# Kernel tuning notes

Hardware: AMD Instinct MI355X
Metric: run time of the kernel (lower is better)

## Reference

```python
import jax, jax.numpy as jnp
import numpy as np

N_CODEBOOKS = 4
N_EMBED = 1024
EMBED_DIM = 64
PATCH = 4
BETA = 0.25
EPS = 1e-5
USAGE_W = 0.01


def setup_inputs() -> dict:
    key = jax.random.key(0)
    k1, k2 = jax.random.split(key)
    z = jax.random.normal(k1, (8, 64, 128, 128), dtype=jnp.float32)
    # one EMA codebook per quantizer, initialized ~ randn like torch buffer
    codebooks = jax.random.normal(k2, (N_CODEBOOKS, N_EMBED, EMBED_DIM), dtype=jnp.float32)
    return {"z": z, "codebooks": codebooks}


def _usage_loss(indices, n_embed):
    # negative-entropy penalty on code usage (no gradient path: counts are ints)
    counts = jnp.bincount(indices.reshape(-1), length=n_embed).astype(jnp.float32)
    probs = (counts + EPS) / (counts.sum() + EPS * n_embed)
    entropy = -jnp.sum(probs * jnp.log(probs + EPS))
    return jnp.log(jnp.float32(n_embed)) - entropy


def _ema_quantize(residual, embedding):
    # residual: [N, C, ph, pw], embedding: [n_e, C]; eval mode (no EMA buffer update)
    N, C, ph, pw = residual.shape
    z_flat = residual.transpose(0, 2, 3, 1).reshape(-1, C)  # [M, C]
    d = (jnp.sum(z_flat ** 2, axis=1, keepdims=True)
         + jnp.sum(embedding ** 2, axis=1)
         - 2.0 * z_flat @ embedding.T)  # [M, n_e]
    idx = jnp.argmin(d, axis=1)  # [M]
    z_q = embedding[idx].reshape(N, ph, pw, C).transpose(0, 3, 1, 2)  # [N, C, ph, pw]
    loss = BETA * jnp.mean((jax.lax.stop_gradient(z_q) - residual) ** 2)
    z_q_st = residual + jax.lax.stop_gradient(z_q - residual)  # straight-through
    return z_q_st, loss, idx.reshape(N, ph, pw)


def reference(z, codebooks):
    B, C, H, W = z.shape
    h, w = H // PATCH, W // PATCH
    # b c (h ph) (w pw) -> (b h w) c ph pw
    zp = (z.reshape(B, C, h, PATCH, w, PATCH)
            .transpose(0, 2, 4, 1, 3, 5)
            .reshape(B * h * w, C, PATCH, PATCH))
    zq_acc = jnp.zeros_like(zp)
    residual = zp
    losses, all_idx = [], []
    for i in range(N_CODEBOOKS):
        zq_i, loss_i, idx_i = _ema_quantize(residual, codebooks[i])
        loss_i = loss_i + USAGE_W * _usage_loss(idx_i, N_EMBED)
        zq_acc = zq_acc + zq_i
        residual = residual - zq_i
        losses.append(loss_i)
        all_idx.append(idx_i.reshape(idx_i.shape[0], -1))  # [N, ph*pw]
    loss = jnp.stack(losses).sum()
    # (b h w) c ph pw -> b c (h ph) (w pw)
    z_q = (zq_acc.reshape(B, h, w, C, PATCH, PATCH)
                 .transpose(0, 3, 1, 4, 2, 5)
                 .reshape(B, C, H, W))
    # [N, patch_area, n_codebooks] -> [b, h, w, patch_area, n_codebooks]
    min_idx = jnp.stack(all_idx, axis=-1).reshape(B, h, w, PATCH * PATCH, N_CODEBOOKS)
    return z_q, loss, min_idx
```

## Files before the change

kernel.cpp:

```cpp
#include <hip/hip_runtime.h>
#include <math.h>

typedef __attribute__((ext_vector_type(8))) short short8;
typedef __attribute__((ext_vector_type(4))) float f32x4;

#define NCB 4
#define NE 1024
#define DIM 64
#define HW 16384
#define NPIX 131072
#define NWAVES 4096
#define MSE_DENOM 8388608.0f
#define EPSF 1e-5f

__device__ __forceinline__ unsigned short f2bf(float x) {
    unsigned u = __float_as_uint(x);
    u += 0x7fffu + ((u >> 16) & 1u);
    return (unsigned short)(u >> 16);
}
__device__ __forceinline__ float bf2f(unsigned short h) {
    return __uint_as_float(((unsigned)h) << 16);
}

__global__ __launch_bounds__(64) void rvq_norms(const float* __restrict__ cb,
                                                float* __restrict__ norms) {
    int code = blockIdx.x * 64 + threadIdx.x;
    const float4* row = reinterpret_cast<const float4*>(cb + (size_t)code * DIM);
    float s0 = 0.f, s1 = 0.f, s2 = 0.f, s3 = 0.f;
#pragma unroll
    for (int k = 0; k < 16; ++k) {
        float4 v = row[k];
        s0 = fmaf(v.x, v.x, s0); s1 = fmaf(v.y, v.y, s1);
        s2 = fmaf(v.z, v.z, s2); s3 = fmaf(v.w, v.w, s3);
    }
    norms[code] = (s0 + s1) + (s2 + s3);
}

__global__ __launch_bounds__(256, 2) void rvq_main(
    const float* __restrict__ z, const float* __restrict__ cb,
    const float* __restrict__ norms,
    float* __restrict__ out_zq, float* __restrict__ out_idx,
    unsigned* __restrict__ hist, float* __restrict__ msePartial)
{
    __shared__ unsigned short sB[3 * 4096];
    __shared__ float sN[64];
    __shared__ int   sBest[4][32];

    const int tid  = threadIdx.x;
    const int lane = tid & 63;
    const int wid  = tid >> 6;
    const int col  = lane & 15;
    const int g    = lane >> 4;
    const int blockPix = blockIdx.x * 128;
    char* sBc = reinterpret_cast<char*>(sB);

    int pf[2]; size_t zb[2];
#pragma unroll
    for (int m = 0; m < 2; ++m) {
        pf[m] = blockPix + wid * 32 + m * 16 + col;
        zb[m] = (size_t)(pf[m] >> 14) * 1048576 + (size_t)(pf[m] & 16383);
    }

    float r[2][2][8];
#pragma unroll
    for (int m = 0; m < 2; ++m)
#pragma unroll
        for (int kh = 0; kh < 2; ++kh)
#pragma unroll
            for (int e = 0; e < 8; ++e)
                r[m][kh][e] = z[zb[m] + (size_t)(kh * 32 + g * 8 + e) * HW];

    for (int i = 0; i < NCB; ++i) {
        const float* cbi = cb + (size_t)i * NE * DIM;

        short8 A[3][2][2];
#pragma unroll
        for (int m = 0; m < 2; ++m)
#pragma unroll
            for (int kh = 0; kh < 2; ++kh)
#pragma unroll
                for (int e = 0; e < 8; ++e) {
                    float t = r[m][kh][e];
                    unsigned short u1 = f2bf(t); t -= bf2f(u1);
                    unsigned short u2 = f2bf(t); t -= bf2f(u2);
                    unsigned short u3 = f2bf(t);
                    A[0][m][kh][e] = (short)u1;
                    A[1][m][kh][e] = (short)u2;
                    A[2][m][kh][e] = (short)u3;
                }

        float minv[2][4]; int mini[2][4];
#pragma unroll
        for (int m = 0; m < 2; ++m)
#pragma unroll
            for (int rr = 0; rr < 4; ++rr) { minv[m][rr] = 3.4e38f; mini[m][rr] = 0; }

        for (int c0 = 0; c0 < NE; c0 += 64) {
            __syncthreads();
            {
                int code = tid >> 2, dg = tid & 3;
                const float4* s4 = reinterpret_cast<const float4*>(
                    cbi + (size_t)(c0 + code) * DIM + dg * 16);
                float v[16];
                {
                    float4 q;
                    q = s4[0]; v[0]=q.x; v[1]=q.y; v[2]=q.z; v[3]=q.w;
                    q = s4[1]; v[4]=q.x; v[5]=q.y; v[6]=q.z; v[7]=q.w;
                    q = s4[2]; v[8]=q.x; v[9]=q.y; v[10]=q.z; v[11]=q.w;
                    q = s4[3]; v[12]=q.x; v[13]=q.y; v[14]=q.z; v[15]=q.w;
                }
                int linbase = code * 128 + dg * 32;
                int sw = (code & 7) << 4;
#pragma unroll
                for (int h = 0; h < 2; ++h) {
                    short8 p1, p2, p3;
#pragma unroll
                    for (int e = 0; e < 8; ++e) {
                        float t = v[h * 8 + e];
                        unsigned short u1 = f2bf(t); t -= bf2f(u1);
                        unsigned short u2 = f2bf(t); t -= bf2f(u2);
                        unsigned short u3 = f2bf(t);
                        p1[e] = (short)u1; p2[e] = (short)u2; p3[e] = (short)u3;
                    }
                    int a = (linbase + h * 16) ^ sw;
                    *reinterpret_cast<short8*>(sBc + a)         = p1;
                    *reinterpret_cast<short8*>(sBc + 8192 + a)  = p2;
                    *reinterpret_cast<short8*>(sBc + 16384 + a) = p3;
                }
                if (tid < 64) sN[tid] = norms[i * NE + c0 + tid];
            }
            __syncthreads();

#pragma unroll
            for (int sub = 0; sub < 4; ++sub) {
                int code = sub * 16 + col;
                int sw = (code & 7) << 4;
                short8 B[3][2];
#pragma unroll
                for (int s = 0; s < 3; ++s)
#pragma unroll
                    for (int kh = 0; kh < 2; ++kh) {
                        int a = ((code << 7) + (kh << 6) + (g << 4)) ^ sw;
                        B[s][kh] = *reinterpret_cast<const short8*>(sBc + s * 8192 + a);
                    }
                float nrm = sN[code];
                f32x4 acc[2][2];
#pragma unroll
                for (int m = 0; m < 2; ++m)
#pragma unroll
                    for (int rr = 0; rr < 4; ++rr) {
                        acc[m][0][rr] = -0.5f * nrm;
                        acc[m][1][rr] = 0.f;
                    }
#pragma unroll
                for (int m = 0; m < 2; ++m)
#pragma unroll
                    for (int kh = 0; kh < 2; ++kh) {
                        acc[m][kh] = __builtin_amdgcn_mfma_f32_16x16x32_bf16(A[0][m][kh], B[0][kh], acc[m][kh], 0, 0, 0);
                        acc[m][kh] = __builtin_amdgcn_mfma_f32_16x16x32_bf16(A[0][m][kh], B[1][kh], acc[m][kh], 0, 0, 0);
                        acc[m][kh] = __builtin_amdgcn_mfma_f32_16x16x32_bf16(A[1][m][kh], B[0][kh], acc[m][kh], 0, 0, 0);
                        acc[m][kh] = __builtin_amdgcn_mfma_f32_16x16x32_bf16(A[0][m][kh], B[2][kh], acc[m][kh], 0, 0, 0);
                        acc[m][kh] = __builtin_amdgcn_mfma_f32_16x16x32_bf16(A[1][m][kh], B[1][kh], acc[m][kh], 0, 0, 0);
                        acc[m][kh] = __builtin_amdgcn_mfma_f32_16x16x32_bf16(A[2][m][kh], B[0][kh], acc[m][kh], 0, 0, 0);
                    }
#pragma unroll
                for (int m = 0; m < 2; ++m)
#pragma unroll
                    for (int rr = 0; rr < 4; ++rr) {
                        float dist = -2.0f * (acc[m][0][rr] + acc[m][1][rr]);
                        if (dist < minv[m][rr]) { minv[m][rr] = dist; mini[m][rr] = c0 + code; }
                    }
            }
        }

#pragma unroll
        for (int m = 0; m < 2; ++m)
#pragma unroll
            for (int rr = 0; rr < 4; ++rr) {
                float v = minv[m][rr]; int ix = mini[m][rr];
#pragma unroll
                for (int off = 1; off < 16; off <<= 1) {
                    float ov = __shfl_xor(v, off, 64);
                    int   oi = __shfl_xor(ix, off, 64);
                    if (ov < v || (ov == v && oi < ix)) { v = ov; ix = oi; }
                }
                minv[m][rr] = v; mini[m][rr] = ix;
            }
        __syncthreads();
        if (col == 0) {
#pragma unroll
            for (int m = 0; m < 2; ++m)
#pragma unroll
                for (int rr = 0; rr < 4; ++rr)
                    sBest[wid][m * 16 + g * 4 + rr] = mini[m][rr];
        }
        __syncthreads();
        int best[2];
        best[0] = sBest[wid][col];
        best[1] = sBest[wid][16 + col];

        if (lane < 16) {
#pragma unroll
            for (int m = 0; m < 2; ++m) {
                int pfr = blockPix + wid * 32 + m * 16 + lane;
                int bb = pfr >> 14, yy = (pfr >> 7) & 127, xx = pfr & 127;
                int bi = sBest[wid][m * 16 + lane];
                size_t off = (size_t)bb * 65536 + (size_t)(yy >> 2) * 2048
                           + (size_t)(xx >> 2) * 64
                           + (size_t)(((yy & 3) << 2) + (xx & 3)) * 4 + (size_t)i;
                out_idx[off] = (float)bi;
                atomicAdd(&hist[i * NE + bi], 1u);
            }
        }

#pragma unroll
        for (int m = 0; m < 2; ++m) {
            const float* er = cbi + (size_t)best[m] * DIM;
#pragma unroll
            for (int kh = 0; kh < 2; ++kh) {
                const float4* e4 = reinterpret_cast<const float4*>(er + kh * 32 + g * 8);
                float4 q0 = e4[0], q1 = e4[1];
                r[m][kh][0] -= q0.x; r[m][kh][1] -= q0.y;
                r[m][kh][2] -= q0.z; r[m][kh][3] -= q0.w;
                r[m][kh][4] -= q1.x; r[m][kh][5] -= q1.y;
                r[m][kh][6] -= q1.z; r[m][kh][7] -= q1.w;
            }
        }

        float s = 0.f;
#pragma unroll
        for (int m = 0; m < 2; ++m)
#pragma unroll
            for (int kh = 0; kh < 2; ++kh)
#pragma unroll
                for (int e = 0; e < 8; ++e) s = fmaf(r[m][kh][e], r[m][kh][e], s);
#pragma unroll
        for (int d_ = 32; d_ > 0; d_ >>= 1) s += __shfl_down(s, d_, 64);
        if (lane == 0) msePartial[i * NWAVES + blockIdx.x * 4 + wid] = s;
    }

#pragma unroll
    for (int m = 0; m < 2; ++m)
#pragma unroll
        for (int kh = 0; kh < 2; ++kh)
#pragma unroll
            for (int e = 0; e < 8; ++e) {
                size_t o = zb[m] + (size_t)(kh * 32 + g * 8 + e) * HW;
                out_zq[o] = z[o] - r[m][kh][e];
            }
}

__global__ __launch_bounds__(1024) void rvq_finalize(
    const unsigned* __restrict__ hist, const float* __restrict__ msePartial,
    float* __restrict__ out_loss)
{
    __shared__ float red[1024];
    int t = threadIdx.x;
    float loss = 0.f;
    for (int i = 0; i < NCB; ++i) {
        float cnt = (float)hist[i * NE + t];
        float prob = (cnt + EPSF) / (131072.0f + EPSF * 1024.0f);
        red[t] = -prob * logf(prob + EPSF);
        __syncthreads();
        for (int s = 512; s > 0; s >>= 1) { if (t < s) red[t] += red[t + s]; __syncthreads(); }
        float entropy = red[0];
        __syncthreads();
        red[t] = msePartial[i * NWAVES + t]        + msePartial[i * NWAVES + 1024 + t]
               + msePartial[i * NWAVES + 2048 + t] + msePartial[i * NWAVES + 3072 + t];
        __syncthreads();
        for (int s = 512; s > 0; s >>= 1) { if (t < s) red[t] += red[t + s]; __syncthreads(); }
        float mse_sum = red[0];
        __syncthreads();
        loss += 0.25f * (mse_sum / MSE_DENOM) + 0.01f * (logf(1024.0f) - entropy);
    }
    if (t == 0) out_loss[0] = loss;
}

extern "C" void kernel_launch(void* const* d_in, const int* in_sizes, int n_in,
                              void* d_out, int out_size, void* d_ws, size_t ws_size,
                              hipStream_t stream) {
    const float* z  = (const float*)d_in[0];
    const float* cb = (const float*)d_in[1];

    float* out      = (float*)d_out;
    float* out_zq   = out;
    float* out_loss = out + 8388608;
    float* out_idx  = out + 8388609;

    unsigned* hist       = (unsigned*)d_ws;
    float*    norms      = (float*)((char*)d_ws + 16384);
    float*    msePartial = (float*)((char*)d_ws + 32768);

    hipMemsetAsync(d_ws, 0, 16384, stream);
    rvq_norms<<<64, 64, 0, stream>>>(cb, norms);
    rvq_main<<<1024, 256, 0, stream>>>(z, cb, norms, out_zq, out_idx, hist, msePartial);
    rvq_finalize<<<1, 1024, 0, stream>>>(hist, msePartial, out_loss);
}
```

Measured before the change: 458.8 us.

## Pre-split codebook into bf16 triplets once and double-buffer chunks in LDS

A new pre-pass kernel converts each codebook into three-way bf16 split form in swizzled chunk layout in workspace, so the main kernel no longer redoes the float-to-bf16x3 split for every block. The main kernel copies these prebuilt chunks from global memory into a double-buffered LDS area, prefetching the next chunk into registers while computing on the current one. Norms are pre-scaled by -0.5 and read directly from global memory, and the argmin over distance becomes an argmax over the score. This adds a kernel launch, extra workspace traffic and doubled LDS, which could lower occupancy.

```diff
diff --git a/kernel.cpp b/kernel.cpp
--- a/kernel.cpp
+++ b/kernel.cpp
@@ -12,6 +12,8 @@
 #define NWAVES 4096
 #define MSE_DENOM 8388608.0f
 #define EPSF 1e-5f
+#define CHUNK_BYTES 24576
+#define CHUNK_SHORTS 12288
 
 __device__ __forceinline__ unsigned short f2bf(float x) {
     unsigned u = __float_as_uint(x);
@@ -23,7 +25,7 @@
 }
 
 __global__ __launch_bounds__(64) void rvq_norms(const float* __restrict__ cb,
-                                                float* __restrict__ norms) {
+                                                float* __restrict__ nrmh) {
     int code = blockIdx.x * 64 + threadIdx.x;
     const float4* row = reinterpret_cast<const float4*>(cb + (size_t)code * DIM);
     float s0 = 0.f, s1 = 0.f, s2 = 0.f, s3 = 0.f;
@@ -33,17 +35,54 @@
         s0 = fmaf(v.x, v.x, s0); s1 = fmaf(v.y, v.y, s1);
         s2 = fmaf(v.z, v.z, s2); s3 = fmaf(v.w, v.w, s3);
     }
-    norms[code] = (s0 + s1) + (s2 + s3);
+    nrmh[code] = -0.5f * ((s0 + s1) + (s2 + s3));
+}
+
+__global__ __launch_bounds__(256) void rvq_presplit(const float* __restrict__ cb,
+                                                    unsigned short* __restrict__ gB) {
+    int blk = blockIdx.x;
+    int tid = threadIdx.x;
+    int code = tid >> 2, dg = tid & 3;
+    int c0 = (blk & 15) << 6;
+    int i  = blk >> 4;
+    const float4* s4 = reinterpret_cast<const float4*>(
+        cb + ((size_t)i * NE + c0 + code) * DIM + dg * 16);
+    float v[16];
+    {
+        float4 q;
+        q = s4[0]; v[0]=q.x; v[1]=q.y; v[2]=q.z; v[3]=q.w;
+        q = s4[1]; v[4]=q.x; v[5]=q.y; v[6]=q.z; v[7]=q.w;
+        q = s4[2]; v[8]=q.x; v[9]=q.y; v[10]=q.z; v[11]=q.w;
+        q = s4[3]; v[12]=q.x; v[13]=q.y; v[14]=q.z; v[15]=q.w;
+    }
+    char* outc = reinterpret_cast<char*>(gB + (size_t)blk * CHUNK_SHORTS);
+    int linbase = code * 128 + dg * 32;
+    int sw = (code & 7) << 4;
+#pragma unroll
+    for (int h = 0; h < 2; ++h) {
+        short8 p1, p2, p3;
+#pragma unroll
+        for (int e = 0; e < 8; ++e) {
+            float t = v[h * 8 + e];
+            unsigned short u1 = f2bf(t); t -= bf2f(u1);
+            unsigned short u2 = f2bf(t); t -= bf2f(u2);
+            unsigned short u3 = f2bf(t);
+            p1[e] = (short)u1; p2[e] = (short)u2; p3[e] = (short)u3;
+        }
+        int a = (linbase + h * 16) ^ sw;
+        *reinterpret_cast<short8*>(outc + a)         = p1;
+        *reinterpret_cast<short8*>(outc + 8192 + a)  = p2;
+        *reinterpret_cast<short8*>(outc + 16384 + a) = p3;
+    }
 }
 
 __global__ __launch_bounds__(256, 2) void rvq_main(
-    const float* __restrict__ z, const float* __restrict__ cb,
-    const float* __restrict__ norms,
+    const float* __restrict__ z, const unsigned short* __restrict__ gB,
+    const float* __restrict__ nrmh, const float* __restrict__ cb,
     float* __restrict__ out_zq, float* __restrict__ out_idx,
     unsigned* __restrict__ hist, float* __restrict__ msePartial)
 {
-    __shared__ unsigned short sB[3 * 4096];
-    __shared__ float sN[64];
+    __shared__ uint4 sB[2][CHUNK_BYTES / 16];
     __shared__ int   sBest[4][32];
 
     const int tid  = threadIdx.x;
@@ -52,7 +91,7 @@
     const int col  = lane & 15;
     const int g    = lane >> 4;
     const int blockPix = blockIdx.x * 128;
-    char* sBc = reinterpret_cast<char*>(sB);
+    char* sBase = reinterpret_cast<char*>(sB);
 
     int pf[2]; size_t zb[2];
 #pragma unroll
@@ -71,7 +110,8 @@
                 r[m][kh][e] = z[zb[m] + (size_t)(kh * 32 + g * 8 + e) * HW];
 
     for (int i = 0; i < NCB; ++i) {
-        const float* cbi = cb + (size_t)i * NE * DIM;
+        const char* gBi = reinterpret_cast<const char*>(gB) + (size_t)i * 16 * CHUNK_BYTES;
+        const float* nrm_i = nrmh + i * NE;
 
         short8 A[3][2][2];
 #pragma unroll
@@ -89,51 +129,38 @@
                     A[2][m][kh][e] = (short)u3;
                 }
 
-        float minv[2][4]; int mini[2][4];
+        uint4 st[6];
+#pragma unroll
+        for (int k = 0; k < 6; ++k)
+            st[k] = *reinterpret_cast<const uint4*>(gBi + tid * 16 + k * 4096);
+#pragma unroll
+        for (int k = 0; k < 6; ++k)
+            *reinterpret_cast<uint4*>(sBase + tid * 16 + k * 4096) = st[k];
+        __syncthreads();
+
+        float maxv[2][4]; int maxi[2][4];
 #pragma unroll
         for (int m = 0; m < 2; ++m)
 #pragma unroll
-            for (int rr = 0; rr < 4; ++rr) { minv[m][rr] = 3.4e38f; mini[m][rr] = 0; }
-
-        for (int c0 = 0; c0 < NE; c0 += 64) {
-            __syncthreads();
-            {
-                int code = tid >> 2, dg = tid & 3;
-                const float4* s4 = reinterpret_cast<const float4*>(
-                    cbi + (size_t)(c0 + code) * DIM + dg * 16);
-                float v[16];
-                {
-                    float4 q;
-                    q = s4[0]; v[0]=q.x; v[1]=q.y; v[2]=q.z; v[3]=q.w;
-                    q = s4[1]; v[4]=q.x; v[5]=q.y; v[6]=q.z; v[7]=q.w;
-                    q = s4[2]; v[8]=q.x; v[9]=q.y; v[10]=q.z; v[11]=q.w;
-                    q = s4[3]; v[12]=q.x; v[13]=q.y; v[14]=q.z; v[15]=q.w;
-                }
-                int linbase = code * 128 + dg * 32;
-                int sw = (code & 7) << 4;
-#pragma unroll
-                for (int h = 0; h < 2; ++h) {
-                    short8 p1, p2, p3;
-#pragma unroll
-                    for (int e = 0; e < 8; ++e) {
-                        float t = v[h * 8 + e];
-                        unsigned short u1 = f2bf(t); t -= bf2f(u1);
-                        unsigned short u2 = f2bf(t); t -= bf2f(u2);
-                        unsigned short u3 = f2bf(t);
-                        p1[e] = (short)u1; p2[e] = (short)u2; p3[e] = (short)u3;
-                    }
-                    int a = (linbase + h * 16) ^ sw;
-                    *reinterpret_cast<short8*>(sBc + a)         = p1;
-                    *reinterpret_cast<short8*>(sBc + 8192 + a)  = p2;
-                    *reinterpret_cast<short8*>(sBc + 16384 + a) = p3;
-                }
-                if (tid < 64) sN[tid] = norms[i * NE + c0 + tid];
-            }
-            __syncthreads();
+            for (int rr = 0; rr < 4; ++rr) { maxv[m][rr] = -3.4e38f; maxi[m][rr] = 0; }
+
+        for (int c = 0; c < 16; ++c) {
+            const int cur = c & 1;
+            if (c < 15) {
+                const char* gc = gBi + (size_t)(c + 1) * CHUNK_BYTES;
+#pragma unroll
+                for (int k = 0; k < 6; ++k)
+                    st[k] = *reinterpret_cast<const uint4*>(gc + tid * 16 + k * 4096);
+            }
+            const char* sbc = sBase + cur * CHUNK_BYTES;
+            float nh[4];
+#pragma unroll
+            for (int sub = 0; sub < 4; ++sub)
+                nh[sub] = nrm_i[(c << 6) + (sub << 4) + col];
 
 #pragma unroll
             for (int sub = 0; sub < 4; ++sub) {
-                int code = sub * 16 + col;
+                int code = (sub << 4) + col;
                 int sw = (code & 7) << 4;
                 short8 B[3][2];
 #pragma unroll
@@ -141,15 +168,14 @@
 #pragma unroll
                     for (int kh = 0; kh < 2; ++kh) {
                         int a = ((code << 7) + (kh << 6) + (g << 4)) ^ sw;
-                        B[s][kh] = *reinterpret_cast<const short8*>(sBc + s * 8192 + a);
+                        B[s][kh] = *reinterpret_cast<const short8*>(sbc + s * 8192 + a);
                     }
-                float nrm = sN[code];
                 f32x4 acc[2][2];
 #pragma unroll
                 for (int m = 0; m < 2; ++m)
 #pragma unroll
                     for (int rr = 0; rr < 4; ++rr) {
-                        acc[m][0][rr] = -0.5f * nrm;
+                        acc[m][0][rr] = nh[sub];
                         acc[m][1][rr] = 0.f;
                     }
 #pragma unroll
@@ -167,24 +193,32 @@
                 for (int m = 0; m < 2; ++m)
 #pragma unroll
                     for (int rr = 0; rr < 4; ++rr) {
-                        float dist = -2.0f * (acc[m][0][rr] + acc[m][1][rr]);
-                        if (dist < minv[m][rr]) { minv[m][rr] = dist; mini[m][rr] = c0 + code; }
+                        float s = acc[m][0][rr] + acc[m][1][rr];
+                        if (s > maxv[m][rr]) { maxv[m][rr] = s; maxi[m][rr] = (c << 6) + code; }
                     }
             }
+            __syncthreads();
+            if (c < 15) {
+                char* sbn = sBase + (cur ^ 1) * CHUNK_BYTES;
+#pragma unroll
+                for (int k = 0; k < 6; ++k)
+                    *reinterpret_cast<uint4*>(sbn + tid * 16 + k * 4096) = st[k];
+                __syncthreads();
+            }
         }
 
 #pragma unroll
         for (int m = 0; m < 2; ++m)
 #pragma unroll
             for (int rr = 0; rr < 4; ++rr) {
-                float v = minv[m][rr]; int ix = mini[m][rr];
+                float v = maxv[m][rr]; int ix = maxi[m][rr];
 #pragma unroll
                 for (int off = 1; off < 16; off <<= 1) {
                     float ov = __shfl_xor(v, off, 64);
                     int   oi = __shfl_xor(ix, off, 64);
-                    if (ov < v || (ov == v && oi < ix)) { v = ov; ix = oi; }
+                    if (ov > v || (ov == v && oi < ix)) { v = ov; ix = oi; }
                 }
-                minv[m][rr] = v; mini[m][rr] = ix;
+                maxi[m][rr] = ix;
             }
         __syncthreads();
         if (col == 0) {
@@ -192,13 +226,14 @@
             for (int m = 0; m < 2; ++m)
 #pragma unroll
                 for (int rr = 0; rr < 4; ++rr)
-                    sBest[wid][m * 16 + g * 4 + rr] = mini[m][rr];
+                    sBest[wid][m * 16 + g * 4 + rr] = maxi[m][rr];
         }
         __syncthreads();
         int best[2];
         best[0] = sBest[wid][col];
         best[1] = sBest[wid][16 + col];
 
+        const float* cbi = cb + (size_t)i * NE * DIM;
         if (lane < 16) {
 #pragma unroll
             for (int m = 0; m < 2; ++m) {
@@ -287,12 +322,14 @@
     float* out_loss = out + 8388608;
     float* out_idx  = out + 8388609;
 
-    unsigned* hist       = (unsigned*)d_ws;
-    float*    norms      = (float*)((char*)d_ws + 16384);
-    float*    msePartial = (float*)((char*)d_ws + 32768);
+    unsigned* hist        = (unsigned*)d_ws;
+    float*    nrmh        = (float*)((char*)d_ws + 16384);
+    float*    msePartial  = (float*)((char*)d_ws + 32768);
+    unsigned short* gB    = (unsigned short*)((char*)d_ws + 98304);
 
     hipMemsetAsync(d_ws, 0, 16384, stream);
-    rvq_norms<<<64, 64, 0, stream>>>(cb, norms);
-    rvq_main<<<1024, 256, 0, stream>>>(z, cb, norms, out_zq, out_idx, hist, msePartial);
+    rvq_norms<<<64, 64, 0, stream>>>(cb, nrmh);
+    rvq_presplit<<<64, 256, 0, stream>>>(cb, gB);
+    rvq_main<<<1024, 256, 0, stream>>>(z, gB, nrmh, cb, out_zq, out_idx, hist, msePartial);
     rvq_finalize<<<1, 1024, 0, stream>>>(hist, msePartial, out_loss);
 }
```

Result: slower. 722.8 us (+57.5%).
